# Kernel optimization log

Measured on AMD Instinct MI355X. Metric: run time of the kernel, lower is better.

## Reference

```python
import jax, jax.numpy as jnp
import numpy as np

ALPHA = 0.1  # LeakyReLU negative slope
F_OUT = 128

def _leaky(x):
    return jnp.where(x >= 0, x, ALPHA * x)

def setup_inputs() -> dict:
    key = jax.random.key(0)
    ks = jax.random.split(key, 12)
    B, N, F_IN = 4, 4096, 128
    q = jax.random.normal(ks[0], (B, N, F_IN), jnp.float32)
    k = jax.random.normal(ks[1], (B, N, F_IN), jnp.float32)
    v = jax.random.normal(ks[2], (B, N, F_IN), jnp.float32)
    adj = jax.random.randint(ks[3], (B, N, N), 0, 2, jnp.int32)
    s = 1.0 / np.sqrt(F_IN)
    Wq_w = jax.random.uniform(ks[4], (F_OUT, F_IN), jnp.float32, -s, s)
    Wq_b = jax.random.uniform(ks[5], (F_OUT,), jnp.float32, -s, s)
    Wk_w = jax.random.uniform(ks[6], (F_OUT, F_IN), jnp.float32, -s, s)
    Wk_b = jax.random.uniform(ks[7], (F_OUT,), jnp.float32, -s, s)
    Wv_w = jax.random.uniform(ks[8], (F_OUT, F_IN), jnp.float32, -s, s)
    Wv_b = jax.random.uniform(ks[9], (F_OUT,), jnp.float32, -s, s)
    # xavier_uniform with gain=1.414 on (2F,1)
    lim = 1.414 * np.sqrt(6.0 / (2 * F_OUT + 1))
    a = jax.random.uniform(ks[10], (2 * F_OUT, 1), jnp.float32, -lim, lim)
    so = 1.0 / np.sqrt(F_OUT)
    Wo_w = jax.random.uniform(ks[11], (F_OUT, F_OUT), jnp.float32, -so, so)
    return {"q": q, "k": k, "v": v, "adj": adj, "Wq_w": Wq_w, "Wq_b": Wq_b,
            "Wk_w": Wk_w, "Wk_b": Wk_b, "Wv_w": Wv_w, "Wv_b": Wv_b,
            "a": a, "Wo_w": Wo_w}

def reference(q, k, v, adj, Wq_w, Wq_b, Wk_w, Wk_b, Wv_w, Wv_b, a, Wo_w):
    qp = q @ Wq_w.T + Wq_b                      # (B,N,F)
    kp = k @ Wk_w.T + Wk_b
    vp = v @ Wv_w.T + Wv_b
    Wh1 = qp @ a[:F_OUT]                        # (B,N,1)
    Wh2 = kp @ a[F_OUT:]                        # (B,N,1)
    e = _leaky(Wh1 + jnp.swapaxes(Wh2, 1, 2))   # (B,N,N)
    e = jnp.where(adj > 0, e, jnp.float32(-1e9))
    att = jax.nn.softmax(e, axis=-1)
    h = jnp.einsum('bnm,bmf->bnf', att, vp)     # (B,N,F)
    return _leaky(h @ Wo_w.T)
```

## Files before the change

### kernel.cpp

```cpp
#include <hip/hip_runtime.h>


constexpr int B = 4, N = 4096, F = 128;
constexpr int BN = B * N;
constexpr int BK = 64;
constexpr int NIT = N / BK;
#define ALPHA 0.1f

using float4v = __attribute__((ext_vector_type(4))) float;
using short8 = __attribute__((ext_vector_type(8))) short;

__device__ __forceinline__ float leaky(float x) { return x >= 0.f ? x : ALPHA * x; }
__device__ __forceinline__ unsigned short f2bf(float x) {
    unsigned u = __float_as_uint(x);
    u = (u + 0x7FFFu + ((u >> 16) & 1u)) >> 16;
    return (unsigned short)u;
}
__device__ __forceinline__ unsigned pack_bf2(float lo, float hi) {
    unsigned a = __float_as_uint(lo), b2 = __float_as_uint(hi);
    a = a + 0x7FFFu + ((a >> 16) & 1u);
    b2 = b2 + 0x7FFFu + ((b2 >> 16) & 1u);
    return __builtin_amdgcn_perm(b2, a, 0x07060302u);
}

__global__ void k_prep(const float* __restrict__ Wq_w, const float* __restrict__ Wq_b,
                       const float* __restrict__ Wk_w, const float* __restrict__ Wk_b,
                       const float* __restrict__ a, float* __restrict__ c1,
                       float* __restrict__ c2, float* __restrict__ d12) {
    __shared__ float as[2 * F];
    __shared__ float red[2 * F];
    int t = threadIdx.x;
    as[t] = a[t];
    __syncthreads();
    int f = t & 127;
    const float* W = (t < F) ? Wq_w : Wk_w;
    const float* ao = (t < F) ? as : as + F;
    float s = 0.f;
#pragma unroll 8
    for (int o = 0; o < F; o++) s = fmaf(W[o * F + f], ao[o], s);
    if (t < F) c1[f] = s; else c2[f] = s;
    red[t] = (t < F) ? Wq_b[f] * as[f] : Wk_b[f] * as[F + f];
    __syncthreads();
    for (int st = 64; st > 0; st >>= 1) {
        if (f < st) red[t] += red[t + st];
        __syncthreads();
    }
    if (t == 0) d12[0] = red[0];
    if (t == F) d12[1] = red[F];
}

__global__ void k_wh(const float* __restrict__ q, const float* __restrict__ k,
                     const float* __restrict__ c1, const float* __restrict__ c2,
                     const float* __restrict__ d12,
                     float* __restrict__ Wh1, float* __restrict__ Wh2) {
    __shared__ float c1s[F], c2s[F];
    int t = threadIdx.x;
    if (t < F) c1s[t] = c1[t]; else c2s[t - F] = c2[t - F];
    __syncthreads();
    int row = blockIdx.x * 8 + (t >> 5);
    int lane = t & 31;
    float4 q4 = reinterpret_cast<const float4*>(q)[row * 32 + lane];
    float4 k4 = reinterpret_cast<const float4*>(k)[row * 32 + lane];
    float s1 = q4.x * c1s[lane * 4 + 0] + q4.y * c1s[lane * 4 + 1] +
               q4.z * c1s[lane * 4 + 2] + q4.w * c1s[lane * 4 + 3];
    float s2 = k4.x * c2s[lane * 4 + 0] + k4.y * c2s[lane * 4 + 1] +
               k4.z * c2s[lane * 4 + 2] + k4.w * c2s[lane * 4 + 3];
    for (int m = 16; m > 0; m >>= 1) { s1 += __shfl_xor(s1, m); s2 += __shfl_xor(s2, m); }
    if (lane == 0) { Wh1[row] = s1 + d12[0]; Wh2[row] = s2 + d12[1]; }
}

__global__ void k_max2(const float* __restrict__ Wh2, float* __restrict__ M2) {
    int b = blockIdx.x, t = threadIdx.x;
    float m = -1e30f;
    for (int i = t; i < N; i += 256) m = fmaxf(m, Wh2[b * N + i]);
    __shared__ float red[256];
    red[t] = m;
    __syncthreads();
    for (int s = 128; s > 0; s >>= 1) { if (t < s) red[t] = fmaxf(red[t], red[t + s]); __syncthreads(); }
    if (t == 0) M2[b] = red[0];
}

__global__ void k_tab(const float* __restrict__ Wh1, const float* __restrict__ Wh2,
                      const float* __restrict__ M2,
                      float* __restrict__ P1, float* __restrict__ Q1,
                      float* __restrict__ P2, float* __restrict__ Q2) {
    int i = blockIdx.x * 256 + threadIdx.x;
    int b = i >> 12;
    float w1 = Wh1[i], w2 = Wh2[i];
    float mi = leaky(w1 + M2[b]);
    P1[i] = __expf(w1 - mi);
    Q1[i] = __expf(ALPHA * w1 - mi);
    P2[i] = __expf(w2);
    Q2[i] = __expf(ALPHA * w2);
}

__global__ __launch_bounds__(256) void k_vp(const float* __restrict__ v,
                                            const float* __restrict__ Wv_w,
                                            const float* __restrict__ Wv_b,
                                            unsigned short* __restrict__ vpT) {
    __shared__ float vs[32][F];
    __shared__ float Ws[F][129];
    __shared__ unsigned short ts[F][40];
    int t = threadIdx.x;
    int row0g = blockIdx.x * 32;
    int b = row0g >> 12;
    int row0 = row0g & (N - 1);
    {
        const float4* src = reinterpret_cast<const float4*>(v + row0g * F);
        float4* dst = reinterpret_cast<float4*>(&vs[0][0]);
#pragma unroll
        for (int u = 0; u < 4; u++) dst[u * 256 + t] = src[u * 256 + t];
    }
    {
        const float4* src = reinterpret_cast<const float4*>(Wv_w);
#pragma unroll
        for (int u = 0; u < 16; u++) {
            int unit = u * 256 + t;
            int r = unit >> 5, s = unit & 31;
            float4 val = src[unit];
            Ws[r][s * 4 + 0] = val.x; Ws[r][s * 4 + 1] = val.y;
            Ws[r][s * 4 + 2] = val.z; Ws[r][s * 4 + 3] = val.w;
        }
    }
    int f = t & 127, g = t >> 7;
    float bias = Wv_b[f];
    __syncthreads();
    float acc[16];
#pragma unroll
    for (int r = 0; r < 16; r++) acc[r] = bias;
    for (int kk = 0; kk < F; kk++) {
        float wk = Ws[f][kk];
#pragma unroll
        for (int r = 0; r < 16; r++) acc[r] = fmaf(vs[g * 16 + r][kk], wk, acc[r]);
    }
#pragma unroll
    for (int r = 0; r < 16; r++) ts[f][g * 16 + r] = f2bf(acc[r]);
    __syncthreads();
    int fr = t >> 1, hseg = t & 1;
    uint4 d0 = *reinterpret_cast<uint4*>(&ts[fr][hseg * 16]);
    uint4 d1 = *reinterpret_cast<uint4*>(&ts[fr][hseg * 16 + 8]);
    unsigned short* dst = vpT + ((size_t)(b * F + fr) * N + row0 + hseg * 16);
    *reinterpret_cast<uint4*>(dst) = d0;
    *reinterpret_cast<uint4*>(dst + 8) = d1;
}

constexpr int LDS_BS_BYTES = 2 * F * 72 * 2;
constexpr int LDS_LOOP_BYTES = LDS_BS_BYTES + 3 * N * 4;
constexpr int LDS_TAIL_BYTES = 64 * 129 * 4 + F * 129 * 4;
constexpr int LDS_BYTES = LDS_TAIL_BYTES;

__global__ __launch_bounds__(256, 1) void k_attn(
    const unsigned short* __restrict__ vpT, const int* __restrict__ adj,
    const float* __restrict__ Wh1, const float* __restrict__ P1, const float* __restrict__ Q1,
    const float* __restrict__ P2, const float* __restrict__ Q2, const float* __restrict__ Wh2,
    const float* __restrict__ Wo_w, float* __restrict__ out) {
    __shared__ __align__(16) char smem[LDS_BYTES];
    auto bs = reinterpret_cast<unsigned short(*)[F][72]>(smem);
    float* sP2 = reinterpret_cast<float*>(smem + LDS_BS_BYTES);
    float* sQ2 = sP2 + N;
    float* sW2 = sQ2 + N;

    int t = threadIdx.x;
    int idx = blockIdx.x;
    int tile = idx & 63;
    int b = idx >> 6;
    int i0 = tile * 64;
    int widx = t >> 6, lane = t & 63, m = lane & 15, q = lane >> 4;
    int r0 = i0 + widx * 16;

    {
        const float4* gp = reinterpret_cast<const float4*>(P2 + (size_t)b * N);
        const float4* gq = reinterpret_cast<const float4*>(Q2 + (size_t)b * N);
        const float4* gw = reinterpret_cast<const float4*>(Wh2 + (size_t)b * N);
        float4* dp = reinterpret_cast<float4*>(sP2);
        float4* dq = reinterpret_cast<float4*>(sQ2);
        float4* dw = reinterpret_cast<float4*>(sW2);
#pragma unroll
        for (int u = 0; u < 4; u++) {
            dp[u * 256 + t] = gp[u * 256 + t];
            dq[u * 256 + t] = gq[u * 256 + t];
            dw[u * 256 + t] = gw[u * 256 + t];
        }
    }

    int gi0 = b * N + r0 + m;
    float p1a = P1[gi0], q1a = Q1[gi0], t1a = -Wh1[gi0];

    const unsigned short* vb = vpT + (size_t)b * F * N;
    const int* adjbase = adj + (size_t)gi0 * N + q * 8;

    uint4 sreg[4];
    int4 aregA[4], aregB[4];

    auto load_stage = [&](int it) {
#pragma unroll
        for (int u = 0; u < 4; u++) {
            int unit = u * 256 + t;
            int r = unit >> 3, s = unit & 7;
            sreg[u] = *reinterpret_cast<const uint4*>(vb + (size_t)r * N + it * BK + s * 8);
        }
    };
    auto write_stage = [&](int pb) {
#pragma unroll
        for (int u = 0; u < 4; u++) {
            int unit = u * 256 + t;
            int r = unit >> 3, s = unit & 7;
            *reinterpret_cast<uint4*>(&bs[pb][r][s * 8]) = sreg[u];
        }
    };
    auto load_adj = [&](int it, int4* ar) {
#pragma unroll
        for (int kh = 0; kh < 2; kh++) {
            const int* p = adjbase + it * BK + kh * 32;
            ar[kh * 2 + 0] = *reinterpret_cast<const int4*>(p);
            ar[kh * 2 + 1] = *reinterpret_cast<const int4*>(p + 4);
        }
    };

    float4v acc0[8];
#pragma unroll
    for (int nt = 0; nt < 8; nt++) acc0[nt] = (float4v){0.f, 0.f, 0.f, 0.f};
    float den0 = 0.f;

    auto gen_af = [&](const int4& a0, const int4& a1, const float4& x2a, const float4& x2b,
                      const float4& p2a, const float4& p2b, const float4& q2a, const float4& q2b,
                      float p1, float q1, float t1, float& den) -> short8 {
        float w0 = a0.x ? ((x2a.x >= t1) ? p1 * p2a.x : q1 * q2a.x) : 0.f;
        float w1 = a0.y ? ((x2a.y >= t1) ? p1 * p2a.y : q1 * q2a.y) : 0.f;
        float w2 = a0.z ? ((x2a.z >= t1) ? p1 * p2a.z : q1 * q2a.z) : 0.f;
        float w3 = a0.w ? ((x2a.w >= t1) ? p1 * p2a.w : q1 * q2a.w) : 0.f;
        float w4 = a1.x ? ((x2b.x >= t1) ? p1 * p2b.x : q1 * q2b.x) : 0.f;
        float w5 = a1.y ? ((x2b.y >= t1) ? p1 * p2b.y : q1 * q2b.y) : 0.f;
        float w6 = a1.z ? ((x2b.z >= t1) ? p1 * p2b.z : q1 * q2b.z) : 0.f;
        float w7 = a1.w ? ((x2b.w >= t1) ? p1 * p2b.w : q1 * q2b.w) : 0.f;
        den += ((w0 + w1) + (w2 + w3)) + ((w4 + w5) + (w6 + w7));
        union { short8 s; uint4 u; } r;
        r.u.x = pack_bf2(w0, w1); r.u.y = pack_bf2(w2, w3);
        r.u.z = pack_bf2(w4, w5); r.u.w = pack_bf2(w6, w7);
        return r.s;
    };

    auto body = [&](int it, int4* cur, int4* nxt, int pb) {
        if (it + 1 < NIT) {
            load_stage(it + 1);
            load_adj(it + 1, nxt);
        }
#pragma unroll
        for (int kh = 0; kh < 2; kh++) {
            int jl = it * BK + kh * 32 + q * 8;
            float4 x2a = *reinterpret_cast<const float4*>(&sW2[jl]);
            float4 x2b = *reinterpret_cast<const float4*>(&sW2[jl + 4]);
            float4 p2a = *reinterpret_cast<const float4*>(&sP2[jl]);
            float4 p2b = *reinterpret_cast<const float4*>(&sP2[jl + 4]);
            float4 q2a = *reinterpret_cast<const float4*>(&sQ2[jl]);
            float4 q2b = *reinterpret_cast<const float4*>(&sQ2[jl + 4]);
            short8 af0 = gen_af(cur[kh * 2 + 0], cur[kh * 2 + 1], x2a, x2b, p2a, p2b, q2a, q2b,
                                p1a, q1a, t1a, den0);
#pragma unroll
            for (int nt = 0; nt < 8; nt++) {
                short8 bf = *reinterpret_cast<const short8*>(&bs[pb][nt * 16 + m][kh * 32 + q * 8]);
                acc0[nt] = __builtin_amdgcn_mfma_f32_16x16x32_bf16(af0, bf, acc0[nt], 0, 0, 0);
            }
        }
        if (it + 1 < NIT) write_stage(pb ^ 1);
        __syncthreads();
    };

    load_stage(0);
    load_adj(0, aregA);
    write_stage(0);
    __syncthreads();

#pragma unroll 1
    for (int ith = 0; ith < NIT / 2; ith++) {
        body(ith * 2 + 0, aregA, aregB, 0);
        body(ith * 2 + 1, aregB, aregA, 1);
    }

    den0 += __shfl_xor(den0, 16);
    den0 += __shfl_xor(den0, 32);

    float (*hs)[129] = reinterpret_cast<float(*)[129]>(smem);
    float (*Ws)[129] = reinterpret_cast<float(*)[129]>(smem + 64 * 129 * 4);

    {
        const float4* src = reinterpret_cast<const float4*>(Wo_w);
#pragma unroll
        for (int u = 0; u < 16; u++) {
            int unit = u * 256 + t;
            int r = unit >> 5, s = unit & 31;
            float4 val = src[unit];
            Ws[r][s * 4 + 0] = val.x; Ws[r][s * 4 + 1] = val.y;
            Ws[r][s * 4 + 2] = val.z; Ws[r][s * 4 + 3] = val.w;
        }
    }
#pragma unroll
    for (int r = 0; r < 4; r++) {
        float inv = 1.f / __shfl(den0, q * 4 + r);
#pragma unroll
        for (int nt = 0; nt < 8; nt++)
            hs[widx * 16 + q * 4 + r][nt * 16 + m] = acc0[nt][r] * inv;
    }
    __syncthreads();

    int f = t & 127, g = t >> 7;
    float acc[32];
#pragma unroll
    for (int r = 0; r < 32; r++) acc[r] = 0.f;
    for (int kk = 0; kk < F; kk++) {
        float wk = Ws[f][kk];
#pragma unroll
        for (int r = 0; r < 32; r++) acc[r] = fmaf(hs[g * 32 + r][kk], wk, acc[r]);
    }
    size_t obase = (size_t)(b * N + i0 + g * 32) * F + f;
#pragma unroll
    for (int r = 0; r < 32; r++) out[obase + (size_t)r * F] = leaky(acc[r]);
}

extern "C" void kernel_launch(void* const* d_in, const int* in_sizes, int n_in,
                              void* d_out, int out_size, void* d_ws, size_t ws_size,
                              hipStream_t stream) {
    const float* q    = (const float*)d_in[0];
    const float* k    = (const float*)d_in[1];
    const float* v    = (const float*)d_in[2];
    const int*   adj  = (const int*)d_in[3];
    const float* Wq_w = (const float*)d_in[4];
    const float* Wq_b = (const float*)d_in[5];
    const float* Wk_w = (const float*)d_in[6];
    const float* Wk_b = (const float*)d_in[7];
    const float* Wv_w = (const float*)d_in[8];
    const float* Wv_b = (const float*)d_in[9];
    const float* a    = (const float*)d_in[10];
    const float* Wo_w = (const float*)d_in[11];
    float* out = (float*)d_out;
    float* ws = (float*)d_ws;

    unsigned short* vpT = (unsigned short*)ws;
    float* Wh1 = ws + BN * F / 2;
    float* Wh2 = Wh1 + BN;
    float* P1  = Wh2 + BN;
    float* Q1  = P1 + BN;
    float* P2  = Q1 + BN;
    float* Q2  = P2 + BN;
    float* c1  = Q2 + BN;
    float* c2  = c1 + F;
    float* d12 = c2 + F;
    float* M2  = d12 + 2;

    k_prep<<<1, 256, 0, stream>>>(Wq_w, Wq_b, Wk_w, Wk_b, a, c1, c2, d12);
    k_wh<<<BN / 8, 256, 0, stream>>>(q, k, c1, c2, d12, Wh1, Wh2);
    k_max2<<<B, 256, 0, stream>>>(Wh2, M2);
    k_tab<<<BN / 256, 256, 0, stream>>>(Wh1, Wh2, M2, P1, Q1, P2, Q2);
    k_vp<<<BN / 32, 256, 0, stream>>>(v, Wv_w, Wv_b, vpT);
    k_attn<<<B * 64, 256, 0, stream>>>(vpT, adj, Wh1, P1, Q1, P2, Q2, Wh2, Wo_w, out);
}
```

Before: 543.4 us.

## Split attention K dimension across two waves per row tile in 512-thread blocks

Doubles the attention block to 512 threads (8 waves). Each pair of waves takes the same 16-row tile but handles different 32-column halves of each 64-wide K chunk. The two partial accumulators and denominators are combined through LDS before normalization. This raises the number of waves per CU, since only 256 blocks cover 256 CUs, to hide adjacency-load and MFMA latency. The cost is an extra LDS reduction, an extra barrier, and higher register pressure with a 512-thread launch bound.

```diff
diff --git a/kernel.cpp b/kernel.cpp
--- a/kernel.cpp
+++ b/kernel.cpp
@@ -145,11 +145,10 @@
 }
 
 constexpr int LDS_BS_BYTES = 2 * F * 72 * 2;
-constexpr int LDS_LOOP_BYTES = LDS_BS_BYTES + 3 * N * 4;
 constexpr int LDS_TAIL_BYTES = 64 * 129 * 4 + F * 129 * 4;
-constexpr int LDS_BYTES = LDS_TAIL_BYTES;
-
-__global__ __launch_bounds__(256, 1) void k_attn(
+constexpr int LDS_BYTES = LDS_TAIL_BYTES + 512;
+
+__global__ __launch_bounds__(512, 1) void k_attn(
     const unsigned short* __restrict__ vpT, const int* __restrict__ adj,
     const float* __restrict__ Wh1, const float* __restrict__ P1, const float* __restrict__ Q1,
     const float* __restrict__ P2, const float* __restrict__ Q2, const float* __restrict__ Wh2,
@@ -159,6 +158,7 @@
     float* sP2 = reinterpret_cast<float*>(smem + LDS_BS_BYTES);
     float* sQ2 = sP2 + N;
     float* sW2 = sQ2 + N;
+    float* denb = reinterpret_cast<float*>(smem + LDS_TAIL_BYTES);
 
     int t = threadIdx.x;
     int idx = blockIdx.x;
@@ -166,7 +166,9 @@
     int b = idx >> 6;
     int i0 = tile * 64;
     int widx = t >> 6, lane = t & 63, m = lane & 15, q = lane >> 4;
-    int r0 = i0 + widx * 16;
+    int rt = widx >> 1;
+    int kh = widx & 1;
+    int r0 = i0 + rt * 16;
 
     {
         const float4* gp = reinterpret_cast<const float4*>(P2 + (size_t)b * N);
@@ -176,10 +178,10 @@
         float4* dq = reinterpret_cast<float4*>(sQ2);
         float4* dw = reinterpret_cast<float4*>(sW2);
 #pragma unroll
-        for (int u = 0; u < 4; u++) {
-            dp[u * 256 + t] = gp[u * 256 + t];
-            dq[u * 256 + t] = gq[u * 256 + t];
-            dw[u * 256 + t] = gw[u * 256 + t];
+        for (int u = 0; u < 2; u++) {
+            dp[u * 512 + t] = gp[u * 512 + t];
+            dq[u * 512 + t] = gq[u * 512 + t];
+            dw[u * 512 + t] = gw[u * 512 + t];
         }
     }
 
@@ -187,34 +189,31 @@
     float p1a = P1[gi0], q1a = Q1[gi0], t1a = -Wh1[gi0];
 
     const unsigned short* vb = vpT + (size_t)b * F * N;
-    const int* adjbase = adj + (size_t)gi0 * N + q * 8;
-
-    uint4 sreg[4];
-    int4 aregA[4], aregB[4];
+    const int* adjbase = adj + (size_t)gi0 * N + kh * 32 + q * 8;
+
+    uint4 sreg[2];
+    int4 aregA[2], aregB[2];
 
     auto load_stage = [&](int it) {
 #pragma unroll
-        for (int u = 0; u < 4; u++) {
-            int unit = u * 256 + t;
+        for (int u = 0; u < 2; u++) {
+            int unit = u * 512 + t;
             int r = unit >> 3, s = unit & 7;
             sreg[u] = *reinterpret_cast<const uint4*>(vb + (size_t)r * N + it * BK + s * 8);
         }
     };
     auto write_stage = [&](int pb) {
 #pragma unroll
-        for (int u = 0; u < 4; u++) {
-            int unit = u * 256 + t;
+        for (int u = 0; u < 2; u++) {
+            int unit = u * 512 + t;
             int r = unit >> 3, s = unit & 7;
             *reinterpret_cast<uint4*>(&bs[pb][r][s * 8]) = sreg[u];
         }
     };
     auto load_adj = [&](int it, int4* ar) {
-#pragma unroll
-        for (int kh = 0; kh < 2; kh++) {
-            const int* p = adjbase + it * BK + kh * 32;
-            ar[kh * 2 + 0] = *reinterpret_cast<const int4*>(p);
-            ar[kh * 2 + 1] = *reinterpret_cast<const int4*>(p + 4);
-        }
+        const int* p = adjbase + it * BK;
+        ar[0] = *reinterpret_cast<const int4*>(p);
+        ar[1] = *reinterpret_cast<const int4*>(p + 4);
     };
 
     float4v acc0[8];
@@ -245,8 +244,7 @@
             load_stage(it + 1);
             load_adj(it + 1, nxt);
         }
-#pragma unroll
-        for (int kh = 0; kh < 2; kh++) {
+        {
             int jl = it * BK + kh * 32 + q * 8;
             float4 x2a = *reinterpret_cast<const float4*>(&sW2[jl]);
             float4 x2b = *reinterpret_cast<const float4*>(&sW2[jl + 4]);
@@ -254,7 +252,7 @@
             float4 p2b = *reinterpret_cast<const float4*>(&sP2[jl + 4]);
             float4 q2a = *reinterpret_cast<const float4*>(&sQ2[jl]);
             float4 q2b = *reinterpret_cast<const float4*>(&sQ2[jl + 4]);
-            short8 af0 = gen_af(cur[kh * 2 + 0], cur[kh * 2 + 1], x2a, x2b, p2a, p2b, q2a, q2b,
+            short8 af0 = gen_af(cur[0], cur[1], x2a, x2b, p2a, p2b, q2a, q2b,
                                 p1a, q1a, t1a, den0);
 #pragma unroll
             for (int nt = 0; nt < 8; nt++) {
@@ -277,44 +275,59 @@
         body(ith * 2 + 1, aregB, aregA, 1);
     }
 
-    den0 += __shfl_xor(den0, 16);
-    den0 += __shfl_xor(den0, 32);
-
     float (*hs)[129] = reinterpret_cast<float(*)[129]>(smem);
     float (*Ws)[129] = reinterpret_cast<float(*)[129]>(smem + 64 * 129 * 4);
 
     {
         const float4* src = reinterpret_cast<const float4*>(Wo_w);
 #pragma unroll
-        for (int u = 0; u < 16; u++) {
-            int unit = u * 256 + t;
+        for (int u = 0; u < 8; u++) {
+            int unit = u * 512 + t;
             int r = unit >> 5, s = unit & 31;
             float4 val = src[unit];
             Ws[r][s * 4 + 0] = val.x; Ws[r][s * 4 + 1] = val.y;
             Ws[r][s * 4 + 2] = val.z; Ws[r][s * 4 + 3] = val.w;
         }
     }
-#pragma unroll
-    for (int r = 0; r < 4; r++) {
-        float inv = 1.f / __shfl(den0, q * 4 + r);
-#pragma unroll
-        for (int nt = 0; nt < 8; nt++)
-            hs[widx * 16 + q * 4 + r][nt * 16 + m] = acc0[nt][r] * inv;
+
+    den0 += __shfl_xor(den0, 16);
+    den0 += __shfl_xor(den0, 32);
+    if (lane < 16) denb[(rt * 2 + kh) * 16 + m] = den0;
+
+    if (kh == 0) {
+#pragma unroll
+        for (int r = 0; r < 4; r++)
+#pragma unroll
+            for (int nt = 0; nt < 8; nt++)
+                hs[rt * 16 + q * 4 + r][nt * 16 + m] = acc0[nt][r];
+    }
+    __syncthreads();
+    if (kh == 1) {
+#pragma unroll
+        for (int r = 0; r < 4; r++) {
+            float dfull = denb[(rt * 2 + 0) * 16 + q * 4 + r] + denb[(rt * 2 + 1) * 16 + q * 4 + r];
+            float inv = 1.f / dfull;
+#pragma unroll
+            for (int nt = 0; nt < 8; nt++) {
+                int row = rt * 16 + q * 4 + r, col = nt * 16 + m;
+                hs[row][col] = (hs[row][col] + acc0[nt][r]) * inv;
+            }
+        }
     }
     __syncthreads();
 
     int f = t & 127, g = t >> 7;
-    float acc[32];
-#pragma unroll
-    for (int r = 0; r < 32; r++) acc[r] = 0.f;
+    float acc[16];
+#pragma unroll
+    for (int r = 0; r < 16; r++) acc[r] = 0.f;
     for (int kk = 0; kk < F; kk++) {
         float wk = Ws[f][kk];
 #pragma unroll
-        for (int r = 0; r < 32; r++) acc[r] = fmaf(hs[g * 32 + r][kk], wk, acc[r]);
-    }
-    size_t obase = (size_t)(b * N + i0 + g * 32) * F + f;
-#pragma unroll
-    for (int r = 0; r < 32; r++) out[obase + (size_t)r * F] = leaky(acc[r]);
+        for (int r = 0; r < 16; r++) acc[r] = fmaf(hs[g * 16 + r][kk], wk, acc[r]);
+    }
+    size_t obase = (size_t)(b * N + i0 + g * 16) * F + f;
+#pragma unroll
+    for (int r = 0; r < 16; r++) out[obase + (size_t)r * F] = leaky(acc[r]);
 }
 
 extern "C" void kernel_launch(void* const* d_in, const int* in_sizes, int n_in,
@@ -352,5 +365,5 @@
     k_max2<<<B, 256, 0, stream>>>(Wh2, M2);
     k_tab<<<BN / 256, 256, 0, stream>>>(Wh1, Wh2, M2, P1, Q1, P2, Q2);
     k_vp<<<BN / 32, 256, 0, stream>>>(v, Wv_w, Wv_b, vpT);
-    k_attn<<<B * 64, 256, 0, stream>>>(vpT, adj, Wh1, P1, Q1, P2, Q2, Wh2, Wo_w, out);
-}
+    k_attn<<<B * 64, 512, 0, stream>>>(vpT, adj, Wh1, P1, Q1, P2, Q2, Wh2, Wo_w, out);
+}
```

New measurement: 511.0 us. 1.06x faster.
